# Performance work log

Hardware: AMD Instinct MI355X
Metric: run time of the kernel (lower is better)

The kernel has to match this reference:

```python
import jax, jax.numpy as jnp
from jax import lax
import numpy as np

B, H, W, C = 8, 128, 128, 256
NUM_ANCHORS_PER_LOC = 15  # len(scales)=5 * len(ratios)=3


def _conv(x, w, b, padding):
    # NHWC conv, HWIO kernel (matches keras Conv2D)
    y = lax.conv_general_dilated(x, w, window_strides=(1, 1), padding=padding,
                                 dimension_numbers=('NHWC', 'HWIO', 'NHWC'))
    return y + b


def setup_inputs() -> dict:
    key = jax.random.key(0)
    ks = jax.random.split(key, 5)
    std = jnp.float32(0.01)  # TruncatedNormal(0, 0.01) init in original
    x = jax.random.normal(ks[0], (B, H, W, C), jnp.float32)
    w_shared = jax.random.normal(ks[1], (3, 3, C, 512), jnp.float32) * std
    b_shared = jnp.zeros((512,), jnp.float32)
    w_cls = jax.random.normal(ks[2], (1, 1, 512, 2 * NUM_ANCHORS_PER_LOC), jnp.float32) * std
    b_cls = jnp.zeros((2 * NUM_ANCHORS_PER_LOC,), jnp.float32)
    w_reg = jax.random.normal(ks[3], (1, 1, 512, 4 * NUM_ANCHORS_PER_LOC), jnp.float32) * std
    b_reg = jnp.zeros((4 * NUM_ANCHORS_PER_LOC,), jnp.float32)
    return {'x': x, 'w_shared': w_shared, 'b_shared': b_shared,
            'w_cls': w_cls, 'b_cls': b_cls, 'w_reg': w_reg, 'b_reg': b_reg}


def reference(x, w_shared, b_shared, w_cls, b_cls, w_reg, b_reg):
    # shared 3x3 conv + relu6
    shared = jnp.clip(_conv(x, w_shared, b_shared, 'SAME'), 0.0, 6.0)
    # class branch: 1x1 conv -> [B, num_anchors, 2] -> softmax
    cls = _conv(shared, w_cls, b_cls, 'VALID')
    rpn_class_logits = cls.reshape(cls.shape[0], -1, 2)
    rpn_probs = jax.nn.softmax(rpn_class_logits, axis=-1)
    reg = _conv(shared, w_reg, b_reg, 'VALID')
    rpn_deltas = reg.reshape(reg.shape[0], -1, 4)
    return (rpn_class_logits, rpn_probs, rpn_deltas)
```

## Files before the change

### kernel.cpp

```cpp
#include <hip/hip_runtime.h>
#include <stdint.h>


#define HH 128
#define WW 128
#define CIN 256

typedef __attribute__((ext_vector_type(8))) short short8;
typedef __attribute__((ext_vector_type(4))) float f32x4;

#define LDS_B_OFF 66560
#define LDS_TOTAL 132096

static __device__ __forceinline__ unsigned short f2bf(float f) {
    uint32_t u = __float_as_uint(f);
    uint32_t r = (u + 0x7FFFu + ((u >> 16) & 1u)) >> 16;
    return (unsigned short)r;
}

__global__ __launch_bounds__(256) void prep_wk(const float* __restrict__ w,
                                               unsigned short* __restrict__ wk) {
    __shared__ unsigned short t[32][130];
    const int c = blockIdx.x >> 2, nh = blockIdx.x & 3;
    const int dydx = c >> 3, kc = c & 7;
    #pragma unroll
    for (int e = 0; e < 16; ++e) {
        int idx = e * 256 + threadIdx.x;
        int kk = idx >> 7, n0 = idx & 127;
        float v = w[((size_t)(dydx * 256 + kc * 32 + kk)) * 512 + nh * 128 + n0];
        t[kk][n0] = f2bf(v);
    }
    __syncthreads();
    #pragma unroll
    for (int e = 0; e < 16; ++e) {
        int idx = e * 256 + threadIdx.x;
        int n0 = idx >> 5, kk = idx & 31;
        int nf = n0 >> 4, l = n0 & 15;
        int np = ((nf >> 2) << 8) | (nh << 6) | ((nf & 3) << 4) | l;
        int kks = kk ^ (((np >> 1) & 3) << 3);
        wk[(size_t)c * 16384 + (size_t)np * 32 + kks] = t[kk][n0];
    }
}

__global__ __launch_bounds__(256) void prep_wbr(const float* __restrict__ wc,
                                                const float* __restrict__ wr,
                                                unsigned short* __restrict__ wbr) {
    int t = blockIdx.x * 256 + threadIdx.x;
    int n = t >> 9, k = t & 511;
    float v = 0.f;
    if (n < 30) v = wc[k * 30 + n];
    else if (n >= 32 && n < 92) v = wr[k * 60 + (n - 32)];
    wbr[n * 512 + k] = f2bf(v);
}

__global__ __launch_bounds__(512, 2) void rpn_fused(
    const float* __restrict__ x, const unsigned short* __restrict__ wk,
    const float* __restrict__ bsh, const unsigned short* __restrict__ wbr,
    const float* __restrict__ bcls, const float* __restrict__ breg,
    float* __restrict__ out)
{
    extern __shared__ char smem[];
    const int tid = threadIdx.x;
    const int lane = tid & 63;
    const int wid = tid >> 6;
    const int wm = wid >> 2, wn = wid & 3;
    const int l15 = lane & 15, l4 = lane >> 4;
    const int blk = blockIdx.x;
    const int bb = blk >> 7, h = blk & 127;

    const int bofs = (wn * 64 + l15) * 64 + ((l4 * 16) ^ (((l15 >> 1) & 3) << 4));

    f32x4 acc[4][8];
    #pragma unroll
    for (int i = 0; i < 4; ++i)
        #pragma unroll
        for (int j = 0; j < 8; ++j) acc[i][j] = (f32x4){0.f, 0.f, 0.f, 0.f};

#define ISSUE_HALF(hh)                                                            \
    if ((hh) < 144) {                                                             \
        const char* s_ = reinterpret_cast<const char*>(wk) + ((size_t)(hh) << 14) \
                         + tid * 16;                                              \
        char* d_ = smem + LDS_B_OFF + (((hh) & 3) << 14) + tid * 16;              \
        __builtin_amdgcn_global_load_lds(reinterpret_cast<const uint32_t*>(s_),   \
                                         reinterpret_cast<uint32_t*>(d_), 16, 0, 0); \
        __builtin_amdgcn_global_load_lds(reinterpret_cast<const uint32_t*>(s_ + 8192), \
                                         reinterpret_cast<uint32_t*>(d_ + 8192), 16, 0, 0); \
    }

#define WAITV(tt)                                                          \
    if ((tt) <= 140)      asm volatile("s_waitcnt vmcnt(4)" ::: "memory"); \
    else if ((tt) == 141) asm volatile("s_waitcnt vmcnt(2)" ::: "memory"); \
    else                  asm volatile("s_waitcnt vmcnt(0)" ::: "memory");

    ISSUE_HALF(0); ISSUE_HALF(1); ISSUE_HALF(2);

    for (int dy = 0; dy < 3; ++dy) {
        {
            const int hp = h + dy - 1;
            const bool hin = (hp >= 0) && (hp < HH);
            const float* xrow = x + ((size_t)(bb * HH + hp)) * WW * CIN;
            for (int u = tid; u < 130 * 32; u += 512) {
                const int pos = u >> 5, c8 = u & 31;
                const int wc = pos - 1;
                float4 f0 = make_float4(0.f,0.f,0.f,0.f), f1 = make_float4(0.f,0.f,0.f,0.f);
                if (hin && (unsigned)wc < WW) {
                    const float4* p = reinterpret_cast<const float4*>(xrow + (size_t)wc * CIN + c8 * 8);
                    f0 = p[0]; f1 = p[1];
                }
                short8 v;
                v[0]=(short)f2bf(f0.x); v[1]=(short)f2bf(f0.y);
                v[2]=(short)f2bf(f0.z); v[3]=(short)f2bf(f0.w);
                v[4]=(short)f2bf(f1.x); v[5]=(short)f2bf(f1.y);
                v[6]=(short)f2bf(f1.z); v[7]=(short)f2bf(f1.w);
                *reinterpret_cast<short8*>(smem + pos * 512 + ((c8 * 16) ^ ((pos & 7) << 4))) = v;
            }
        }
        if (dy == 0) asm volatile("s_waitcnt vmcnt(4) lgkmcnt(0)" ::: "memory");
        else         asm volatile("s_waitcnt lgkmcnt(0)" ::: "memory");
        __builtin_amdgcn_sched_barrier(0);
        __builtin_amdgcn_s_barrier();

        for (int i = 0; i < 24; ++i) {
            const int g = dy * 24 + i;
            const int t0 = 2 * g;
            const int dx = i >> 3, kc = i & 7;

            const char* slot0 = smem + LDS_B_OFF + ((t0 & 3) << 14);
            const int r0 = wm * 64 + l15 + dx;
            const int asw = ((kc * 32 + l4 * 8) << 1) ^ ((r0 & 7) << 4);
            short8 af0 = *reinterpret_cast<const short8*>(smem + (r0     ) * 512 + asw);
            short8 af1 = *reinterpret_cast<const short8*>(smem + (r0 + 16) * 512 + asw);
            short8 af2 = *reinterpret_cast<const short8*>(smem + (r0 + 32) * 512 + asw);
            short8 af3 = *reinterpret_cast<const short8*>(smem + (r0 + 48) * 512 + asw);
            short8 b0 = *reinterpret_cast<const short8*>(slot0 + bofs);
            short8 b1 = *reinterpret_cast<const short8*>(slot0 + bofs + 1024);
            short8 b2 = *reinterpret_cast<const short8*>(slot0 + bofs + 2048);
            short8 b3 = *reinterpret_cast<const short8*>(slot0 + bofs + 3072);
            ISSUE_HALF(t0 + 3);
            WAITV(t0);
            __builtin_amdgcn_s_barrier();
            asm volatile("s_waitcnt lgkmcnt(0)" ::: "memory");
            __builtin_amdgcn_sched_barrier(0);
            __builtin_amdgcn_s_setprio(1);
            acc[0][0] = __builtin_amdgcn_mfma_f32_16x16x32_bf16(af0, b0, acc[0][0], 0, 0, 0);
            acc[1][0] = __builtin_amdgcn_mfma_f32_16x16x32_bf16(af1, b0, acc[1][0], 0, 0, 0);
            acc[2][0] = __builtin_amdgcn_mfma_f32_16x16x32_bf16(af2, b0, acc[2][0], 0, 0, 0);
            acc[3][0] = __builtin_amdgcn_mfma_f32_16x16x32_bf16(af3, b0, acc[3][0], 0, 0, 0);
            acc[0][1] = __builtin_amdgcn_mfma_f32_16x16x32_bf16(af0, b1, acc[0][1], 0, 0, 0);
            acc[1][1] = __builtin_amdgcn_mfma_f32_16x16x32_bf16(af1, b1, acc[1][1], 0, 0, 0);
            acc[2][1] = __builtin_amdgcn_mfma_f32_16x16x32_bf16(af2, b1, acc[2][1], 0, 0, 0);
            acc[3][1] = __builtin_amdgcn_mfma_f32_16x16x32_bf16(af3, b1, acc[3][1], 0, 0, 0);
            acc[0][2] = __builtin_amdgcn_mfma_f32_16x16x32_bf16(af0, b2, acc[0][2], 0, 0, 0);
            acc[1][2] = __builtin_amdgcn_mfma_f32_16x16x32_bf16(af1, b2, acc[1][2], 0, 0, 0);
            acc[2][2] = __builtin_amdgcn_mfma_f32_16x16x32_bf16(af2, b2, acc[2][2], 0, 0, 0);
            acc[3][2] = __builtin_amdgcn_mfma_f32_16x16x32_bf16(af3, b2, acc[3][2], 0, 0, 0);
            acc[0][3] = __builtin_amdgcn_mfma_f32_16x16x32_bf16(af0, b3, acc[0][3], 0, 0, 0);
            acc[1][3] = __builtin_amdgcn_mfma_f32_16x16x32_bf16(af1, b3, acc[1][3], 0, 0, 0);
            acc[2][3] = __builtin_amdgcn_mfma_f32_16x16x32_bf16(af2, b3, acc[2][3], 0, 0, 0);
            acc[3][3] = __builtin_amdgcn_mfma_f32_16x16x32_bf16(af3, b3, acc[3][3], 0, 0, 0);
            __builtin_amdgcn_s_setprio(0);
            __builtin_amdgcn_s_barrier();

            const char* slot1 = smem + LDS_B_OFF + (((t0 + 1) & 3) << 14);
            short8 b4 = *reinterpret_cast<const short8*>(slot1 + bofs);
            short8 b5 = *reinterpret_cast<const short8*>(slot1 + bofs + 1024);
            short8 b6 = *reinterpret_cast<const short8*>(slot1 + bofs + 2048);
            short8 b7 = *reinterpret_cast<const short8*>(slot1 + bofs + 3072);
            ISSUE_HALF(t0 + 4);
            WAITV(t0 + 1);
            __builtin_amdgcn_s_barrier();
            asm volatile("s_waitcnt lgkmcnt(0)" ::: "memory");
            __builtin_amdgcn_sched_barrier(0);
            __builtin_amdgcn_s_setprio(1);
            acc[0][4] = __builtin_amdgcn_mfma_f32_16x16x32_bf16(af0, b4, acc[0][4], 0, 0, 0);
            acc[1][4] = __builtin_amdgcn_mfma_f32_16x16x32_bf16(af1, b4, acc[1][4], 0, 0, 0);
            acc[2][4] = __builtin_amdgcn_mfma_f32_16x16x32_bf16(af2, b4, acc[2][4], 0, 0, 0);
            acc[3][4] = __builtin_amdgcn_mfma_f32_16x16x32_bf16(af3, b4, acc[3][4], 0, 0, 0);
            acc[0][5] = __builtin_amdgcn_mfma_f32_16x16x32_bf16(af0, b5, acc[0][5], 0, 0, 0);
            acc[1][5] = __builtin_amdgcn_mfma_f32_16x16x32_bf16(af1, b5, acc[1][5], 0, 0, 0);
            acc[2][5] = __builtin_amdgcn_mfma_f32_16x16x32_bf16(af2, b5, acc[2][5], 0, 0, 0);
            acc[3][5] = __builtin_amdgcn_mfma_f32_16x16x32_bf16(af3, b5, acc[3][5], 0, 0, 0);
            acc[0][6] = __builtin_amdgcn_mfma_f32_16x16x32_bf16(af0, b6, acc[0][6], 0, 0, 0);
            acc[1][6] = __builtin_amdgcn_mfma_f32_16x16x32_bf16(af1, b6, acc[1][6], 0, 0, 0);
            acc[2][6] = __builtin_amdgcn_mfma_f32_16x16x32_bf16(af2, b6, acc[2][6], 0, 0, 0);
            acc[3][6] = __builtin_amdgcn_mfma_f32_16x16x32_bf16(af3, b6, acc[3][6], 0, 0, 0);
            acc[0][7] = __builtin_amdgcn_mfma_f32_16x16x32_bf16(af0, b7, acc[0][7], 0, 0, 0);
            acc[1][7] = __builtin_amdgcn_mfma_f32_16x16x32_bf16(af1, b7, acc[1][7], 0, 0, 0);
            acc[2][7] = __builtin_amdgcn_mfma_f32_16x16x32_bf16(af2, b7, acc[2][7], 0, 0, 0);
            acc[3][7] = __builtin_amdgcn_mfma_f32_16x16x32_bf16(af3, b7, acc[3][7], 0, 0, 0);
            __builtin_amdgcn_s_setprio(0);
            __builtin_amdgcn_s_barrier();
        }
    }

    __syncthreads();
    #pragma unroll
    for (int nf = 0; nf < 8; ++nf) {
        const int ch = wn * 128 + nf * 16 + l15;
        const float bv = bsh[ch];
        #pragma unroll
        for (int mf = 0; mf < 4; ++mf) {
            #pragma unroll
            for (int r = 0; r < 4; ++r) {
                const int pos = wm * 64 + mf * 16 + l4 * 4 + r;
                float v = acc[mf][nf][r] + bv;
                v = fminf(fmaxf(v, 0.f), 6.f);
                *reinterpret_cast<unsigned short*>(
                    smem + pos * 1024 + ((ch * 2) ^ ((pos & 7) << 4))) = f2bf(v);
            }
        }
    }
    __syncthreads();

    f32x4 bacc[6];
    #pragma unroll
    for (int nf = 0; nf < 6; ++nf) bacc[nf] = (f32x4){0.f,0.f,0.f,0.f};
    const int pos0 = wid * 16;
    #pragma unroll 4
    for (int kstep = 0; kstep < 16; ++kstep) {
        const int ch = kstep * 32 + l4 * 8;
        const int posr = pos0 + l15;
        short8 af = *reinterpret_cast<const short8*>(
            smem + posr * 1024 + ((ch * 2) ^ ((posr & 7) << 4)));
        #pragma unroll
        for (int nf = 0; nf < 6; ++nf) {
            const int n = nf * 16 + l15;
            short8 bfr = *reinterpret_cast<const short8*>(wbr + n * 512 + ch);
            bacc[nf] = __builtin_amdgcn_mfma_f32_16x16x32_bf16(af, bfr, bacc[nf], 0, 0, 0);
        }
    }

    const size_t rowbase = (size_t)h * 128;
    #pragma unroll
    for (int nf = 0; nf < 2; ++nf) {
        const int n = nf * 16 + l15;
        const float bias = (n < 30) ? bcls[n] : 0.f;
        #pragma unroll
        for (int r = 0; r < 4; ++r) {
            float v = bacc[nf][r] + bias;
            float vo = __shfl_xor(v, 1);
            float mx = fmaxf(v, vo);
            float e  = __expf(v - mx), eo = __expf(vo - mx);
            float p  = e / (e + eo);
            if (n < 30) {
                const int wc = pos0 + l4 * 4 + r;
                const size_t anchor = (rowbase + wc) * 15 + (n >> 1);
                const size_t idx = (size_t)bb * 491520 + anchor * 2 + (n & 1);
                out[idx] = v;
                out[3932160 + idx] = p;
            }
        }
    }
    #pragma unroll
    for (int nf = 2; nf < 6; ++nf) {
        const int n = nf * 16 + l15;
        const int nr = n - 32;
        const float bias = (nr < 60) ? breg[nr] : 0.f;
        #pragma unroll
        for (int r = 0; r < 4; ++r) {
            float v = bacc[nf][r] + bias;
            if (nr < 60) {
                const int wc = pos0 + l4 * 4 + r;
                const size_t anchor = (rowbase + wc) * 15 + (nr >> 2);
                out[7864320 + (size_t)bb * 983040 + anchor * 4 + (nr & 3)] = v;
            }
        }
    }
}

extern "C" void kernel_launch(void* const* d_in, const int* in_sizes, int n_in,
                              void* d_out, int out_size, void* d_ws, size_t ws_size,
                              hipStream_t stream) {
    const float* x    = (const float*)d_in[0];
    const float* wsh  = (const float*)d_in[1];
    const float* bsh  = (const float*)d_in[2];
    const float* wcls = (const float*)d_in[3];
    const float* bcls = (const float*)d_in[4];
    const float* wreg = (const float*)d_in[5];
    const float* breg = (const float*)d_in[6];
    float* out = (float*)d_out;

    unsigned short* wk  = (unsigned short*)d_ws;
    unsigned short* wbr = wk + 1179648;

    prep_wk <<<288, 256, 0, stream>>>(wsh, wk);
    prep_wbr<<<192, 256, 0, stream>>>(wcls, wreg, wbr);

    hipFuncSetAttribute((const void*)rpn_fused,
                        hipFuncAttributeMaxDynamicSharedMemorySize, LDS_TOTAL);
    rpn_fused<<<1024, 512, LDS_TOTAL, stream>>>(x, wk, bsh, wbr, bcls, breg, out);
}
```

Baseline: 611.8 us.

## Split rows in half per block, reorder K by channel chunks, shrink LDS for occupancy

Each block now computes 64 output positions of one row instead of 128. The K loop is reordered so each step stages a 64-channel slice of the input row in a small LDS tile and streams 32KB weight chunks through a two-slot ring. The weight prep kernel is changed to emit this new chunk order. LDS per block drops to roughly 74KB and the launch bound asks for more resident blocks, aiming for better latency hiding and more blocks in flight. In exchange, each weight chunk is now reused by only 64 positions, so global weight traffic doubles, and input rows are converted and restaged 12 times per block.

```diff
diff --git a/kernel.cpp b/kernel.cpp
--- a/kernel.cpp
+++ b/kernel.cpp
@@ -9,8 +9,8 @@
 typedef __attribute__((ext_vector_type(8))) short short8;
 typedef __attribute__((ext_vector_type(4))) float f32x4;
 
-#define LDS_B_OFF 66560
-#define LDS_TOTAL 132096
+#define SLOT_OFF 8448
+#define LDS_TOTAL 73984
 
 static __device__ __forceinline__ unsigned short f2bf(float f) {
     uint32_t u = __float_as_uint(f);
@@ -22,12 +22,14 @@
                                                unsigned short* __restrict__ wk) {
     __shared__ unsigned short t[32][130];
     const int c = blockIdx.x >> 2, nh = blockIdx.x & 3;
-    const int dydx = c >> 3, kc = c & 7;
+    const int dydx = c >> 3, kcg = c & 7;
+    const int dy = dydx / 3, dx = dydx - dy * 3;
+    const int q = (kcg >> 1) * 18 + dy * 6 + dx * 2 + (kcg & 1);
     #pragma unroll
     for (int e = 0; e < 16; ++e) {
         int idx = e * 256 + threadIdx.x;
         int kk = idx >> 7, n0 = idx & 127;
-        float v = w[((size_t)(dydx * 256 + kc * 32 + kk)) * 512 + nh * 128 + n0];
+        float v = w[((size_t)(dydx * 256 + kcg * 32 + kk)) * 512 + nh * 128 + n0];
         t[kk][n0] = f2bf(v);
     }
     __syncthreads();
@@ -35,10 +37,9 @@
     for (int e = 0; e < 16; ++e) {
         int idx = e * 256 + threadIdx.x;
         int n0 = idx >> 5, kk = idx & 31;
-        int nf = n0 >> 4, l = n0 & 15;
-        int np = ((nf >> 2) << 8) | (nh << 6) | ((nf & 3) << 4) | l;
-        int kks = kk ^ (((np >> 1) & 3) << 3);
-        wk[(size_t)c * 16384 + (size_t)np * 32 + kks] = t[kk][n0];
+        int n = nh * 128 + n0;
+        int kks = kk ^ (((n >> 1) & 3) << 3);
+        wk[(size_t)q * 16384 + (size_t)n * 32 + kks] = t[kk][n0];
     }
 }
 
@@ -53,7 +54,7 @@
     wbr[n * 512 + k] = f2bf(v);
 }
 
-__global__ __launch_bounds__(512, 2) void rpn_fused(
+__global__ __launch_bounds__(512, 4) void rpn_fused(
     const float* __restrict__ x, const unsigned short* __restrict__ wk,
     const float* __restrict__ bsh, const unsigned short* __restrict__ wbr,
     const float* __restrict__ bcls, const float* __restrict__ breg,
@@ -63,159 +64,128 @@
     const int tid = threadIdx.x;
     const int lane = tid & 63;
     const int wid = tid >> 6;
-    const int wm = wid >> 2, wn = wid & 3;
     const int l15 = lane & 15, l4 = lane >> 4;
     const int blk = blockIdx.x;
-    const int bb = blk >> 7, h = blk & 127;
-
-    const int bofs = (wn * 64 + l15) * 64 + ((l4 * 16) ^ (((l15 >> 1) & 3) << 4));
-
-    f32x4 acc[4][8];
+    const int bb = blk >> 8, h = (blk >> 1) & 127, mh = blk & 1;
+
+    const int bofs = (wid * 64 + l15) * 64 + ((l4 * 16) ^ (((l15 >> 1) & 3) << 4));
+
+    f32x4 acc[4][4];
     #pragma unroll
     for (int i = 0; i < 4; ++i)
         #pragma unroll
-        for (int j = 0; j < 8; ++j) acc[i][j] = (f32x4){0.f, 0.f, 0.f, 0.f};
-
-#define ISSUE_HALF(hh)                                                            \
-    if ((hh) < 144) {                                                             \
-        const char* s_ = reinterpret_cast<const char*>(wk) + ((size_t)(hh) << 14) \
-                         + tid * 16;                                              \
-        char* d_ = smem + LDS_B_OFF + (((hh) & 3) << 14) + tid * 16;              \
-        __builtin_amdgcn_global_load_lds(reinterpret_cast<const uint32_t*>(s_),   \
-                                         reinterpret_cast<uint32_t*>(d_), 16, 0, 0); \
-        __builtin_amdgcn_global_load_lds(reinterpret_cast<const uint32_t*>(s_ + 8192), \
-                                         reinterpret_cast<uint32_t*>(d_ + 8192), 16, 0, 0); \
-    }
-
-#define WAITV(tt)                                                          \
-    if ((tt) <= 140)      asm volatile("s_waitcnt vmcnt(4)" ::: "memory"); \
-    else if ((tt) == 141) asm volatile("s_waitcnt vmcnt(2)" ::: "memory"); \
-    else                  asm volatile("s_waitcnt vmcnt(0)" ::: "memory");
-
-    ISSUE_HALF(0); ISSUE_HALF(1); ISSUE_HALF(2);
-
-    for (int dy = 0; dy < 3; ++dy) {
-        {
-            const int hp = h + dy - 1;
-            const bool hin = (hp >= 0) && (hp < HH);
-            const float* xrow = x + ((size_t)(bb * HH + hp)) * WW * CIN;
-            for (int u = tid; u < 130 * 32; u += 512) {
-                const int pos = u >> 5, c8 = u & 31;
-                const int wc = pos - 1;
-                float4 f0 = make_float4(0.f,0.f,0.f,0.f), f1 = make_float4(0.f,0.f,0.f,0.f);
-                if (hin && (unsigned)wc < WW) {
-                    const float4* p = reinterpret_cast<const float4*>(xrow + (size_t)wc * CIN + c8 * 8);
-                    f0 = p[0]; f1 = p[1];
+        for (int j = 0; j < 4; ++j) acc[i][j] = (f32x4){0.f, 0.f, 0.f, 0.f};
+
+#define ISSUE_CHUNK(qq) do {                                                       \
+    const char* s_ = reinterpret_cast<const char*>(wk) + ((size_t)(qq) << 15)      \
+                     + tid * 16;                                                   \
+    char* d_ = smem + SLOT_OFF + (((qq) & 1) << 15) + tid * 16;                    \
+    __builtin_amdgcn_global_load_lds(reinterpret_cast<const uint32_t*>(s_),        \
+                                     reinterpret_cast<uint32_t*>(d_), 16, 0, 0);   \
+    __builtin_amdgcn_global_load_lds(reinterpret_cast<const uint32_t*>(s_ + 8192), \
+                                     reinterpret_cast<uint32_t*>(d_ + 8192), 16, 0, 0); \
+    __builtin_amdgcn_global_load_lds(reinterpret_cast<const uint32_t*>(s_ + 16384),\
+                                     reinterpret_cast<uint32_t*>(d_ + 16384), 16, 0, 0); \
+    __builtin_amdgcn_global_load_lds(reinterpret_cast<const uint32_t*>(s_ + 24576),\
+                                     reinterpret_cast<uint32_t*>(d_ + 24576), 16, 0, 0); \
+} while (0)
+
+    ISSUE_CHUNK(0);
+
+    int t = 0;
+    for (int q4 = 0; q4 < 4; ++q4) {
+        for (int dy = 0; dy < 3; ++dy) {
+            {
+                const int hp = h + dy - 1;
+                const bool hin = (hp >= 0) && (hp < HH);
+                const float* xrow = x + ((size_t)(bb * HH + hp)) * WW * CIN + q4 * 64;
+                for (int u = tid; u < 66 * 8; u += 512) {
+                    const int pos = u >> 3, c8 = u & 7;
+                    const int wc = mh * 64 + pos - 1;
+                    float4 f0 = make_float4(0.f,0.f,0.f,0.f), f1 = make_float4(0.f,0.f,0.f,0.f);
+                    if (hin && (unsigned)wc < WW) {
+                        const float4* p = reinterpret_cast<const float4*>(xrow + (size_t)wc * CIN + c8 * 8);
+                        f0 = p[0]; f1 = p[1];
+                    }
+                    short8 v;
+                    v[0]=(short)f2bf(f0.x); v[1]=(short)f2bf(f0.y);
+                    v[2]=(short)f2bf(f0.z); v[3]=(short)f2bf(f0.w);
+                    v[4]=(short)f2bf(f1.x); v[5]=(short)f2bf(f1.y);
+                    v[6]=(short)f2bf(f1.z); v[7]=(short)f2bf(f1.w);
+                    *reinterpret_cast<short8*>(smem + pos * 128 + ((c8 * 16) ^ ((pos & 7) << 4))) = v;
                 }
-                short8 v;
-                v[0]=(short)f2bf(f0.x); v[1]=(short)f2bf(f0.y);
-                v[2]=(short)f2bf(f0.z); v[3]=(short)f2bf(f0.w);
-                v[4]=(short)f2bf(f1.x); v[5]=(short)f2bf(f1.y);
-                v[6]=(short)f2bf(f1.z); v[7]=(short)f2bf(f1.w);
-                *reinterpret_cast<short8*>(smem + pos * 512 + ((c8 * 16) ^ ((pos & 7) << 4))) = v;
-            }
-        }
-        if (dy == 0) asm volatile("s_waitcnt vmcnt(4) lgkmcnt(0)" ::: "memory");
-        else         asm volatile("s_waitcnt lgkmcnt(0)" ::: "memory");
-        __builtin_amdgcn_sched_barrier(0);
-        __builtin_amdgcn_s_barrier();
-
-        for (int i = 0; i < 24; ++i) {
-            const int g = dy * 24 + i;
-            const int t0 = 2 * g;
-            const int dx = i >> 3, kc = i & 7;
-
-            const char* slot0 = smem + LDS_B_OFF + ((t0 & 3) << 14);
-            const int r0 = wm * 64 + l15 + dx;
-            const int asw = ((kc * 32 + l4 * 8) << 1) ^ ((r0 & 7) << 4);
-            short8 af0 = *reinterpret_cast<const short8*>(smem + (r0     ) * 512 + asw);
-            short8 af1 = *reinterpret_cast<const short8*>(smem + (r0 + 16) * 512 + asw);
-            short8 af2 = *reinterpret_cast<const short8*>(smem + (r0 + 32) * 512 + asw);
-            short8 af3 = *reinterpret_cast<const short8*>(smem + (r0 + 48) * 512 + asw);
-            short8 b0 = *reinterpret_cast<const short8*>(slot0 + bofs);
-            short8 b1 = *reinterpret_cast<const short8*>(slot0 + bofs + 1024);
-            short8 b2 = *reinterpret_cast<const short8*>(slot0 + bofs + 2048);
-            short8 b3 = *reinterpret_cast<const short8*>(slot0 + bofs + 3072);
-            ISSUE_HALF(t0 + 3);
-            WAITV(t0);
-            __builtin_amdgcn_s_barrier();
+            }
             asm volatile("s_waitcnt lgkmcnt(0)" ::: "memory");
             __builtin_amdgcn_sched_barrier(0);
-            __builtin_amdgcn_s_setprio(1);
-            acc[0][0] = __builtin_amdgcn_mfma_f32_16x16x32_bf16(af0, b0, acc[0][0], 0, 0, 0);
-            acc[1][0] = __builtin_amdgcn_mfma_f32_16x16x32_bf16(af1, b0, acc[1][0], 0, 0, 0);
-            acc[2][0] = __builtin_amdgcn_mfma_f32_16x16x32_bf16(af2, b0, acc[2][0], 0, 0, 0);
-            acc[3][0] = __builtin_amdgcn_mfma_f32_16x16x32_bf16(af3, b0, acc[3][0], 0, 0, 0);
-            acc[0][1] = __builtin_amdgcn_mfma_f32_16x16x32_bf16(af0, b1, acc[0][1], 0, 0, 0);
-            acc[1][1] = __builtin_amdgcn_mfma_f32_16x16x32_bf16(af1, b1, acc[1][1], 0, 0, 0);
-            acc[2][1] = __builtin_amdgcn_mfma_f32_16x16x32_bf16(af2, b1, acc[2][1], 0, 0, 0);
-            acc[3][1] = __builtin_amdgcn_mfma_f32_16x16x32_bf16(af3, b1, acc[3][1], 0, 0, 0);
-            acc[0][2] = __builtin_amdgcn_mfma_f32_16x16x32_bf16(af0, b2, acc[0][2], 0, 0, 0);
-            acc[1][2] = __builtin_amdgcn_mfma_f32_16x16x32_bf16(af1, b2, acc[1][2], 0, 0, 0);
-            acc[2][2] = __builtin_amdgcn_mfma_f32_16x16x32_bf16(af2, b2, acc[2][2], 0, 0, 0);
-            acc[3][2] = __builtin_amdgcn_mfma_f32_16x16x32_bf16(af3, b2, acc[3][2], 0, 0, 0);
-            acc[0][3] = __builtin_amdgcn_mfma_f32_16x16x32_bf16(af0, b3, acc[0][3], 0, 0, 0);
-            acc[1][3] = __builtin_amdgcn_mfma_f32_16x16x32_bf16(af1, b3, acc[1][3], 0, 0, 0);
-            acc[2][3] = __builtin_amdgcn_mfma_f32_16x16x32_bf16(af2, b3, acc[2][3], 0, 0, 0);
-            acc[3][3] = __builtin_amdgcn_mfma_f32_16x16x32_bf16(af3, b3, acc[3][3], 0, 0, 0);
-            __builtin_amdgcn_s_setprio(0);
             __builtin_amdgcn_s_barrier();
 
-            const char* slot1 = smem + LDS_B_OFF + (((t0 + 1) & 3) << 14);
-            short8 b4 = *reinterpret_cast<const short8*>(slot1 + bofs);
-            short8 b5 = *reinterpret_cast<const short8*>(slot1 + bofs + 1024);
-            short8 b6 = *reinterpret_cast<const short8*>(slot1 + bofs + 2048);
-            short8 b7 = *reinterpret_cast<const short8*>(slot1 + bofs + 3072);
-            ISSUE_HALF(t0 + 4);
-            WAITV(t0 + 1);
-            __builtin_amdgcn_s_barrier();
-            asm volatile("s_waitcnt lgkmcnt(0)" ::: "memory");
-            __builtin_amdgcn_sched_barrier(0);
-            __builtin_amdgcn_s_setprio(1);
-            acc[0][4] = __builtin_amdgcn_mfma_f32_16x16x32_bf16(af0, b4, acc[0][4], 0, 0, 0);
-            acc[1][4] = __builtin_amdgcn_mfma_f32_16x16x32_bf16(af1, b4, acc[1][4], 0, 0, 0);
-            acc[2][4] = __builtin_amdgcn_mfma_f32_16x16x32_bf16(af2, b4, acc[2][4], 0, 0, 0);
-            acc[3][4] = __builtin_amdgcn_mfma_f32_16x16x32_bf16(af3, b4, acc[3][4], 0, 0, 0);
-            acc[0][5] = __builtin_amdgcn_mfma_f32_16x16x32_bf16(af0, b5, acc[0][5], 0, 0, 0);
-            acc[1][5] = __builtin_amdgcn_mfma_f32_16x16x32_bf16(af1, b5, acc[1][5], 0, 0, 0);
-            acc[2][5] = __builtin_amdgcn_mfma_f32_16x16x32_bf16(af2, b5, acc[2][5], 0, 0, 0);
-            acc[3][5] = __builtin_amdgcn_mfma_f32_16x16x32_bf16(af3, b5, acc[3][5], 0, 0, 0);
-            acc[0][6] = __builtin_amdgcn_mfma_f32_16x16x32_bf16(af0, b6, acc[0][6], 0, 0, 0);
-            acc[1][6] = __builtin_amdgcn_mfma_f32_16x16x32_bf16(af1, b6, acc[1][6], 0, 0, 0);
-            acc[2][6] = __builtin_amdgcn_mfma_f32_16x16x32_bf16(af2, b6, acc[2][6], 0, 0, 0);
-            acc[3][6] = __builtin_amdgcn_mfma_f32_16x16x32_bf16(af3, b6, acc[3][6], 0, 0, 0);
-            acc[0][7] = __builtin_amdgcn_mfma_f32_16x16x32_bf16(af0, b7, acc[0][7], 0, 0, 0);
-            acc[1][7] = __builtin_amdgcn_mfma_f32_16x16x32_bf16(af1, b7, acc[1][7], 0, 0, 0);
-            acc[2][7] = __builtin_amdgcn_mfma_f32_16x16x32_bf16(af2, b7, acc[2][7], 0, 0, 0);
-            acc[3][7] = __builtin_amdgcn_mfma_f32_16x16x32_bf16(af3, b7, acc[3][7], 0, 0, 0);
-            __builtin_amdgcn_s_setprio(0);
-            __builtin_amdgcn_s_barrier();
+            for (int i = 0; i < 6; ++i, ++t) {
+                const int dx = i >> 1, kc2 = i & 1;
+                const int r0 = l15 + dx;
+                const int chh = kc2 * 32 + l4 * 8;
+                const int asw = (chh * 2) ^ ((r0 & 7) << 4);
+                short8 af0 = *reinterpret_cast<const short8*>(smem + (r0     ) * 128 + asw);
+                short8 af1 = *reinterpret_cast<const short8*>(smem + (r0 + 16) * 128 + asw);
+                short8 af2 = *reinterpret_cast<const short8*>(smem + (r0 + 32) * 128 + asw);
+                short8 af3 = *reinterpret_cast<const short8*>(smem + (r0 + 48) * 128 + asw);
+                if (t + 1 < 72) ISSUE_CHUNK(t + 1);
+                if (t < 71) asm volatile("s_waitcnt vmcnt(4)" ::: "memory");
+                else        asm volatile("s_waitcnt vmcnt(0)" ::: "memory");
+                __builtin_amdgcn_s_barrier();
+                const char* slot = smem + SLOT_OFF + ((t & 1) << 15);
+                short8 b0 = *reinterpret_cast<const short8*>(slot + bofs);
+                short8 b1 = *reinterpret_cast<const short8*>(slot + bofs + 1024);
+                short8 b2 = *reinterpret_cast<const short8*>(slot + bofs + 2048);
+                short8 b3 = *reinterpret_cast<const short8*>(slot + bofs + 3072);
+                asm volatile("s_waitcnt lgkmcnt(0)" ::: "memory");
+                __builtin_amdgcn_sched_barrier(0);
+                __builtin_amdgcn_s_setprio(1);
+                acc[0][0] = __builtin_amdgcn_mfma_f32_16x16x32_bf16(af0, b0, acc[0][0], 0, 0, 0);
+                acc[1][0] = __builtin_amdgcn_mfma_f32_16x16x32_bf16(af1, b0, acc[1][0], 0, 0, 0);
+                acc[2][0] = __builtin_amdgcn_mfma_f32_16x16x32_bf16(af2, b0, acc[2][0], 0, 0, 0);
+                acc[3][0] = __builtin_amdgcn_mfma_f32_16x16x32_bf16(af3, b0, acc[3][0], 0, 0, 0);
+                acc[0][1] = __builtin_amdgcn_mfma_f32_16x16x32_bf16(af0, b1, acc[0][1], 0, 0, 0);
+                acc[1][1] = __builtin_amdgcn_mfma_f32_16x16x32_bf16(af1, b1, acc[1][1], 0, 0, 0);
+                acc[2][1] = __builtin_amdgcn_mfma_f32_16x16x32_bf16(af2, b1, acc[2][1], 0, 0, 0);
+                acc[3][1] = __builtin_amdgcn_mfma_f32_16x16x32_bf16(af3, b1, acc[3][1], 0, 0, 0);
+                acc[0][2] = __builtin_amdgcn_mfma_f32_16x16x32_bf16(af0, b2, acc[0][2], 0, 0, 0);
+                acc[1][2] = __builtin_amdgcn_mfma_f32_16x16x32_bf16(af1, b2, acc[1][2], 0, 0, 0);
+                acc[2][2] = __builtin_amdgcn_mfma_f32_16x16x32_bf16(af2, b2, acc[2][2], 0, 0, 0);
+                acc[3][2] = __builtin_amdgcn_mfma_f32_16x16x32_bf16(af3, b2, acc[3][2], 0, 0, 0);
+                acc[0][3] = __builtin_amdgcn_mfma_f32_16x16x32_bf16(af0, b3, acc[0][3], 0, 0, 0);
+                acc[1][3] = __builtin_amdgcn_mfma_f32_16x16x32_bf16(af1, b3, acc[1][3], 0, 0, 0);
+                acc[2][3] = __builtin_amdgcn_mfma_f32_16x16x32_bf16(af2, b3, acc[2][3], 0, 0, 0);
+                acc[3][3] = __builtin_amdgcn_mfma_f32_16x16x32_bf16(af3, b3, acc[3][3], 0, 0, 0);
+                __builtin_amdgcn_s_setprio(0);
+                __builtin_amdgcn_s_barrier();
+            }
         }
     }
 
     __syncthreads();
     #pragma unroll
-    for (int nf = 0; nf < 8; ++nf) {
-        const int ch = wn * 128 + nf * 16 + l15;
-        const float bv = bsh[ch];
+    for (int nf = 0; nf < 4; ++nf) {
+        const int n = wid * 64 + nf * 16 + l15;
+        const float bv = bsh[n];
         #pragma unroll
         for (int mf = 0; mf < 4; ++mf) {
             #pragma unroll
             for (int r = 0; r < 4; ++r) {
-                const int pos = wm * 64 + mf * 16 + l4 * 4 + r;
+                const int pos = mf * 16 + l4 * 4 + r;
                 float v = acc[mf][nf][r] + bv;
                 v = fminf(fmaxf(v, 0.f), 6.f);
                 *reinterpret_cast<unsigned short*>(
-                    smem + pos * 1024 + ((ch * 2) ^ ((pos & 7) << 4))) = f2bf(v);
+                    smem + pos * 1024 + ((n * 2) ^ ((pos & 7) << 4))) = f2bf(v);
             }
         }
     }
     __syncthreads();
 
-    f32x4 bacc[6];
-    #pragma unroll
-    for (int nf = 0; nf < 6; ++nf) bacc[nf] = (f32x4){0.f,0.f,0.f,0.f};
-    const int pos0 = wid * 16;
+    f32x4 bacc[3];
+    #pragma unroll
+    for (int j = 0; j < 3; ++j) bacc[j] = (f32x4){0.f,0.f,0.f,0.f};
+    const int pos0 = (wid & 3) * 16;
+    const int nf_off = (wid >> 2) * 3;
     #pragma unroll 4
     for (int kstep = 0; kstep < 16; ++kstep) {
         const int ch = kstep * 32 + l4 * 8;
@@ -223,46 +193,46 @@
         short8 af = *reinterpret_cast<const short8*>(
             smem + posr * 1024 + ((ch * 2) ^ ((posr & 7) << 4)));
         #pragma unroll
-        for (int nf = 0; nf < 6; ++nf) {
-            const int n = nf * 16 + l15;
+        for (int j = 0; j < 3; ++j) {
+            const int n = (nf_off + j) * 16 + l15;
             short8 bfr = *reinterpret_cast<const short8*>(wbr + n * 512 + ch);
-            bacc[nf] = __builtin_amdgcn_mfma_f32_16x16x32_bf16(af, bfr, bacc[nf], 0, 0, 0);
+            bacc[j] = __builtin_amdgcn_mfma_f32_16x16x32_bf16(af, bfr, bacc[j], 0, 0, 0);
         }
     }
 
     const size_t rowbase = (size_t)h * 128;
     #pragma unroll
-    for (int nf = 0; nf < 2; ++nf) {
+    for (int j = 0; j < 3; ++j) {
+        const int nf = nf_off + j;
         const int n = nf * 16 + l15;
-        const float bias = (n < 30) ? bcls[n] : 0.f;
-        #pragma unroll
-        for (int r = 0; r < 4; ++r) {
-            float v = bacc[nf][r] + bias;
-            float vo = __shfl_xor(v, 1);
-            float mx = fmaxf(v, vo);
-            float e  = __expf(v - mx), eo = __expf(vo - mx);
-            float p  = e / (e + eo);
-            if (n < 30) {
-                const int wc = pos0 + l4 * 4 + r;
-                const size_t anchor = (rowbase + wc) * 15 + (n >> 1);
-                const size_t idx = (size_t)bb * 491520 + anchor * 2 + (n & 1);
-                out[idx] = v;
-                out[3932160 + idx] = p;
-            }
-        }
-    }
-    #pragma unroll
-    for (int nf = 2; nf < 6; ++nf) {
-        const int n = nf * 16 + l15;
-        const int nr = n - 32;
-        const float bias = (nr < 60) ? breg[nr] : 0.f;
-        #pragma unroll
-        for (int r = 0; r < 4; ++r) {
-            float v = bacc[nf][r] + bias;
-            if (nr < 60) {
-                const int wc = pos0 + l4 * 4 + r;
-                const size_t anchor = (rowbase + wc) * 15 + (nr >> 2);
-                out[7864320 + (size_t)bb * 983040 + anchor * 4 + (nr & 3)] = v;
+        if (nf < 2) {
+            const float bias = (n < 30) ? bcls[n] : 0.f;
+            #pragma unroll
+            for (int r = 0; r < 4; ++r) {
+                float v = bacc[j][r] + bias;
+                float vo = __shfl_xor(v, 1);
+                float mx = fmaxf(v, vo);
+                float e  = __expf(v - mx), eo = __expf(vo - mx);
+                float p  = e / (e + eo);
+                if (n < 30) {
+                    const int wc = mh * 64 + pos0 + l4 * 4 + r;
+                    const size_t anchor = (rowbase + wc) * 15 + (n >> 1);
+                    const size_t idx = (size_t)bb * 491520 + anchor * 2 + (n & 1);
+                    out[idx] = v;
+                    out[3932160 + idx] = p;
+                }
+            }
+        } else {
+            const int nr = n - 32;
+            const float bias = (nr < 60) ? breg[nr] : 0.f;
+            #pragma unroll
+            for (int r = 0; r < 4; ++r) {
+                float v = bacc[j][r] + bias;
+                if (nr < 60) {
+                    const int wc = mh * 64 + pos0 + l4 * 4 + r;
+                    const size_t anchor = (rowbase + wc) * 15 + (nr >> 2);
+                    out[7864320 + (size_t)bb * 983040 + anchor * 4 + (nr & 3)] = v;
+                }
             }
         }
     }
@@ -288,5 +258,5 @@
 
     hipFuncSetAttribute((const void*)rpn_fused,
                         hipFuncAttributeMaxDynamicSharedMemorySize, LDS_TOTAL);
-    rpn_fused<<<1024, 512, LDS_TOTAL, stream>>>(x, wk, bsh, wbr, bcls, breg, out);
-}
+    rpn_fused<<<2048, 512, LDS_TOTAL, stream>>>(x, wk, bsh, wbr, bcls, breg, out);
+}
```

Result: no change. 607.7 us (-0.7%).
